# Kernel tuning notes

Hardware: AMD Instinct MI355X
Metric: run time of the kernel (lower is better)

The kernel has to match this reference:

```python
import jax, jax.numpy as jnp
import numpy as np

DIM = 1024
NUM_EXPERTS = 8
TOP_K = 2
HIDDEN = DIM * 2
B, S = 2, 4096


def setup_inputs() -> dict:
    key = jax.random.key(0)
    ks = jax.random.split(key, 8)
    sd = 1.0 / np.sqrt(DIM)
    sh = 1.0 / np.sqrt(HIDDEN)
    return {
        "x": jax.random.normal(ks[0], (B, S, DIM), dtype=jnp.float32),
        "gate_w": jax.random.uniform(ks[1], (NUM_EXPERTS, DIM), jnp.float32, -sd, sd),
        "gate_b": jax.random.uniform(ks[2], (NUM_EXPERTS,), jnp.float32, -sd, sd),
        "W1": jax.random.uniform(ks[3], (NUM_EXPERTS, DIM, HIDDEN), jnp.float32, -sd, sd),
        "b1": jax.random.uniform(ks[4], (NUM_EXPERTS, HIDDEN), jnp.float32, -sd, sd),
        "W2": jax.random.uniform(ks[5], (NUM_EXPERTS, HIDDEN, DIM), jnp.float32, -sh, sh),
        "b2": jax.random.uniform(ks[6], (NUM_EXPERTS, DIM), jnp.float32, -sh, sh),
    }


def reference(x, gate_w, gate_b, W1, b1, W2, b2):
    Bd, Sd, D = x.shape
    xf = x.reshape(-1, D)                                  # [T, D]
    T = xf.shape[0]
    logits = xf @ gate_w.T + gate_b                        # [T, E]
    weights = jax.nn.softmax(logits.astype(jnp.float32), axis=-1)
    topk_w, topk_i = jax.lax.top_k(weights, TOP_K)         # [T, K]
    topk_w = topk_w / topk_w.sum(axis=-1, keepdims=True)
    # combine weights scattered back to dense [T, E] (top-k indices are distinct)
    comb = jnp.zeros((T, NUM_EXPERTS), topk_w.dtype)
    comb = comb.at[jnp.arange(T)[:, None], topk_i].add(topk_w)
    # dense all-expert FFN (exact GELU, matching nn.GELU default)
    h = jax.nn.gelu(jnp.einsum('td,edh->eth', xf, W1) + b1[:, None, :], approximate=False)
    y = jnp.einsum('eth,ehd->etd', h, W2) + b2[:, None, :]  # [E, T, D]
    out = jnp.einsum('etd,te->td', y, comb.astype(y.dtype)).reshape(Bd, Sd, D)
    return out, logits
```

## Files before the change

### kernel.cpp

```cpp
#include <hip/hip_runtime.h>
#include <math.h>

#define T_TOK 8192
#define DIMX 1024
#define NE 8
#define HID 2048
#define NPAIR (T_TOK * 2)
#define P_PAD (NPAIR + NE * 128)
#define GATE_TPB 32

typedef __attribute__((ext_vector_type(8))) short s16x8;
typedef __attribute__((ext_vector_type(4))) float f32x4;

static __device__ __forceinline__ unsigned short f2bf(float f) {
    union { float f; unsigned u; } v; v.f = f;
    unsigned r = v.u + 0x7FFFu + ((v.u >> 16) & 1u);
    return (unsigned short)(r >> 16);
}
static __device__ __forceinline__ float bf2f(unsigned short u) {
    union { unsigned u; float f; } v; v.u = (unsigned)u << 16; return v.f;
}

static __device__ __forceinline__ float gelu_fast(float v) {
    float u2 = -1.5957691216057308f * v * (1.f + 0.044715f * v * v);
    return v * __builtin_amdgcn_rcpf(1.f + __expf(u2));
}

static __device__ __forceinline__ void gload16(const unsigned short* g, unsigned short* l) {
    __builtin_amdgcn_global_load_lds(
        (const __attribute__((address_space(1))) unsigned int*)g,
        (__attribute__((address_space(3))) unsigned int*)l, 16, 0, 0);
}

__global__ void init_routing_kernel(int* slot_token, float* slot_weight, int* counts) {
    int i = blockIdx.x * blockDim.x + threadIdx.x;
    if (i < P_PAD) { slot_token[i] = 0; slot_weight[i] = 0.f; }
    if (i < NE) counts[i] = 0;
}

__global__ __launch_bounds__(256) void conv_transpose_kernel(
    const float* __restrict__ src, unsigned short* __restrict__ dst, int R, int C) {
    __shared__ float tile[64][65];
    int e = blockIdx.z;
    int r0 = blockIdx.y * 64, c0 = blockIdx.x * 64;
    const float* s = src + (size_t)e * R * C;
    unsigned short* d = dst + (size_t)e * R * C;
    int tid = threadIdx.x;
    int lr = tid >> 4, lc4 = (tid & 15) * 4;
    #pragma unroll
    for (int it = 0; it < 4; it++) {
        float4 v = *(const float4*)&s[(size_t)(r0 + it * 16 + lr) * C + c0 + lc4];
        tile[it * 16 + lr][lc4 + 0] = v.x;
        tile[it * 16 + lr][lc4 + 1] = v.y;
        tile[it * 16 + lr][lc4 + 2] = v.z;
        tile[it * 16 + lr][lc4 + 3] = v.w;
    }
    __syncthreads();
    int cc = tid >> 3, rch = (tid & 7) * 8;
    #pragma unroll
    for (int it = 0; it < 2; it++) {
        int c = it * 32 + cc;
        unsigned short r[8];
        #pragma unroll
        for (int j = 0; j < 8; j++) r[j] = f2bf(tile[rch + j][c]);
        *(uint4*)&d[(size_t)(c0 + c) * R + r0 + rch] = *(const uint4*)&r[0];
    }
}

__global__ __launch_bounds__(256) void gate_kernel(
    const float* __restrict__ x, const float* __restrict__ gw, const float* __restrict__ gb,
    float* __restrict__ logits_out, int* counts, int* __restrict__ pair_epos,
    float* __restrict__ pair_w, unsigned short* __restrict__ xb) {
    __shared__ float sgw[NE * DIMX];
    __shared__ int lcount[NE], lbase[NE];
    __shared__ int s_e[GATE_TPB * 2];
    __shared__ int s_lp[GATE_TPB * 2];
    __shared__ float s_wv[GATE_TPB * 2];
    int tid = threadIdx.x;
    for (int i = tid; i < NE * DIMX / 4; i += 256)
        ((float4*)sgw)[i] = ((const float4*)gw)[i];
    if (tid < NE) lcount[tid] = 0;
    __syncthreads();

    int wave = tid >> 6, lane = tid & 63;
    int tbase = blockIdx.x * GATE_TPB;
    for (int r = 0; r < GATE_TPB / 4; ++r) {
        int ti = wave * (GATE_TPB / 4) + r;
        int t = tbase + ti;
        const float* xr = x + (size_t)t * DIMX;
        float acc[NE] = {};
        #pragma unroll
        for (int i = 0; i < DIMX / 256; i++) {
            float4 xv = *(const float4*)&xr[i * 256 + lane * 4];
            unsigned short rb[4] = { f2bf(xv.x), f2bf(xv.y), f2bf(xv.z), f2bf(xv.w) };
            *(uint2*)&xb[(size_t)t * DIMX + i * 256 + lane * 4] = *(const uint2*)&rb[0];
            #pragma unroll
            for (int e = 0; e < NE; e++) {
                float4 wv = *(const float4*)&sgw[e * DIMX + i * 256 + lane * 4];
                acc[e] += xv.x * wv.x + xv.y * wv.y + xv.z * wv.z + xv.w * wv.w;
            }
        }
        #pragma unroll
        for (int e = 0; e < NE; e++) {
            #pragma unroll
            for (int off = 32; off; off >>= 1) acc[e] += __shfl_xor(acc[e], off);
        }
        if (lane == 0) {
            float* lo = logits_out + (size_t)t * NE;
            #pragma unroll
            for (int e = 0; e < NE; e++) { acc[e] += gb[e]; lo[e] = acc[e]; }
            float l0 = acc[0]; int e0 = 0;
            #pragma unroll
            for (int e = 1; e < NE; e++) if (acc[e] > l0) { l0 = acc[e]; e0 = e; }
            float l1 = -1e30f; int e1 = -1;
            #pragma unroll
            for (int e = 0; e < NE; e++) if (e != e0 && acc[e] > l1) { l1 = acc[e]; e1 = e; }
            float q = expf(l1 - l0);
            float wn0 = 1.f / (1.f + q);
            float wn1 = q / (1.f + q);
            int lp0 = atomicAdd(&lcount[e0], 1);
            int lp1 = atomicAdd(&lcount[e1], 1);
            s_e[ti * 2] = e0; s_lp[ti * 2] = lp0; s_wv[ti * 2] = wn0;
            s_e[ti * 2 + 1] = e1; s_lp[ti * 2 + 1] = lp1; s_wv[ti * 2 + 1] = wn1;
        }
    }
    __syncthreads();
    if (tid < NE) lbase[tid] = atomicAdd(&counts[tid], lcount[tid]);
    __syncthreads();
    if (tid < GATE_TPB * 2) {
        int e = s_e[tid];
        int gp = lbase[e] + s_lp[tid];
        int gi = (tbase + (tid >> 1)) * 2 + (tid & 1);
        pair_epos[gi] = (e << 28) | gp;
        pair_w[gi] = s_wv[tid];
    }
}

__global__ void scan_kernel(const int* counts, int* offsets) {
    if (threadIdx.x == 0 && blockIdx.x == 0) {
        int o = 0;
        offsets[0] = 0;
        for (int e = 0; e < NE; e++) { o += (counts[e] + 127) & ~127; offsets[e + 1] = o; }
    }
}

__global__ void place_kernel(const int* __restrict__ pair_epos, const float* __restrict__ pair_w,
                             const int* __restrict__ offsets, int* __restrict__ slot_token,
                             float* __restrict__ slot_weight, int* __restrict__ tok2slot) {
    int p = blockIdx.x * 256 + threadIdx.x;
    if (p >= NPAIR) return;
    int ep = pair_epos[p];
    int e = ep >> 28;
    int pos = ep & 0x0FFFFFFF;
    int slot = offsets[e] + pos;
    slot_token[slot] = p >> 1;
    slot_weight[slot] = pair_w[p];
    tok2slot[p] = slot;
}

#define BARRIER() asm volatile("s_barrier" ::: "memory")
#define WAIT_VM(n) asm volatile("s_waitcnt vmcnt(" #n ")" ::: "memory")
#define WAIT_LGKM0() do { asm volatile("s_waitcnt lgkmcnt(0)" ::: "memory"); \
                          __builtin_amdgcn_sched_barrier(0); } while (0)


__global__ __launch_bounds__(256) void gemm1_kernel(
    const unsigned short* __restrict__ xb, const unsigned short* __restrict__ W1t,
    const float* __restrict__ b1, const int* __restrict__ offsets,
    const int* __restrict__ slot_token, unsigned short* __restrict__ hbuf) {
    int e = blockIdx.x;
    int row_base = offsets[e];
    int rows = offsets[e + 1] - row_base;
    int m0 = blockIdx.z * 128;
    if (m0 >= rows) return;
    int n0 = blockIdx.y * 128;

    __shared__ unsigned short sA[2][128 * 32];
    __shared__ unsigned short sB[2][128 * 32];

    int tid = threadIdx.x;
    const unsigned short* w1e = W1t + (size_t)e * HID * DIMX;

    int srow = tid >> 2;
    int kperm = (tid & 3) ^ ((tid >> 3) & 3);
    int tok0 = slot_token[row_base + m0 + srow];
    int tok1 = slot_token[row_base + m0 + srow + 64];
    const unsigned short* gA0 = xb + (size_t)tok0 * DIMX + kperm * 8;
    const unsigned short* gA1 = xb + (size_t)tok1 * DIMX + kperm * 8;
    const unsigned short* gB0 = w1e + (size_t)(n0 + srow) * DIMX + kperm * 8;
    const unsigned short* gB1 = w1e + (size_t)(n0 + srow + 64) * DIMX + kperm * 8;

#define STG1(b, k0) do { \
        gload16(gA0 + (k0), &sA[b][tid * 8]); \
        gload16(gA1 + (k0), &sA[b][(tid + 256) * 8]); \
        gload16(gB0 + (k0), &sB[b][tid * 8]); \
        gload16(gB1 + (k0), &sB[b][(tid + 256) * 8]); \
    } while (0)

    f32x4 acc[4][4] = {};
    int wv = tid >> 6; int wr = wv >> 1, wc = wv & 1;
    int lane = tid & 63; int lr = lane & 15, lg = lane >> 4;
    int kx8 = (lg ^ ((lr >> 1) & 3)) * 8;

#define CMP1(CUR) do { \
        s16x8 af[4], bfr[4]; \
        _Pragma("unroll") \
        for (int m = 0; m < 4; m++) af[m] = *(const s16x8*)&sA[CUR][(wr * 64 + m * 16 + lr) * 32 + kx8]; \
        _Pragma("unroll") \
        for (int n = 0; n < 4; n++) bfr[n] = *(const s16x8*)&sB[CUR][(wc * 64 + n * 16 + lr) * 32 + kx8]; \
        __builtin_amdgcn_s_setprio(1); \
        _Pragma("unroll") \
        for (int m = 0; m < 4; m++) { \
            _Pragma("unroll") \
            for (int n = 0; n < 4; n++) \
                acc[m][n] = __builtin_amdgcn_mfma_f32_16x16x32_bf16(af[m], bfr[n], acc[m][n], 0, 0, 0); \
        } \
        __builtin_amdgcn_s_setprio(0); \
    } while (0)

    const int NT = DIMX / 32;
    STG1(0, 0);
    int cur = 0;
    for (int t = 0; t < NT - 1; ++t) {
        STG1(cur ^ 1, (t + 1) * 32);
        WAIT_VM(4);
        BARRIER();
        CMP1(cur);
        WAIT_LGKM0();
        BARRIER();
        cur ^= 1;
    }
    WAIT_VM(0);
    BARRIER();
    CMP1(cur);
#undef STG1
#undef CMP1

    #pragma unroll
    for (int m = 0; m < 4; m++) {
        #pragma unroll
        for (int n = 0; n < 4; n++) {
            int col = n0 + wc * 64 + n * 16 + lr;
            float bias = b1[e * HID + col];
            #pragma unroll
            for (int i = 0; i < 4; i++) {
                int row = wr * 64 + m * 16 + lg * 4 + i;
                float v = gelu_fast(acc[m][n][i] + bias);
                hbuf[(size_t)(row_base + m0 + row) * HID + col] = f2bf(v);
            }
        }
    }
}

__global__ __launch_bounds__(256) void gemm2_kernel(
    const unsigned short* __restrict__ hbuf, const unsigned short* __restrict__ W2t,
    const float* __restrict__ b2, const int* __restrict__ offsets,
    const float* __restrict__ slot_weight, unsigned short* __restrict__ ybuf) {
    int e = blockIdx.x;
    int row_base = offsets[e];
    int rows = offsets[e + 1] - row_base;
    int m0 = blockIdx.z * 128;
    if (m0 >= rows) return;
    int n0 = blockIdx.y * 128;

    __shared__ unsigned short sA[2][128 * 32];
    __shared__ unsigned short sB[2][128 * 32];
    __shared__ float s_w[128];

    int tid = threadIdx.x;
    if (tid < 128) s_w[tid] = slot_weight[row_base + m0 + tid];

    const unsigned short* ha = hbuf + (size_t)(row_base + m0) * HID;
    const unsigned short* w2e = W2t + (size_t)e * DIMX * HID;

    int srow = tid >> 2;
    int kperm = (tid & 3) ^ ((tid >> 3) & 3);
    const unsigned short* gA0 = ha + (size_t)srow * HID + kperm * 8;
    const unsigned short* gA1 = ha + (size_t)(srow + 64) * HID + kperm * 8;
    const unsigned short* gB0 = w2e + (size_t)(n0 + srow) * HID + kperm * 8;
    const unsigned short* gB1 = w2e + (size_t)(n0 + srow + 64) * HID + kperm * 8;

#define STG2(b, k0) do { \
        gload16(gA0 + (k0), &sA[b][tid * 8]); \
        gload16(gA1 + (k0), &sA[b][(tid + 256) * 8]); \
        gload16(gB0 + (k0), &sB[b][tid * 8]); \
        gload16(gB1 + (k0), &sB[b][(tid + 256) * 8]); \
    } while (0)

    f32x4 acc[4][4] = {};
    int wv = tid >> 6; int wr = wv >> 1, wc = wv & 1;
    int lane = tid & 63; int lr = lane & 15, lg = lane >> 4;
    int kx8 = (lg ^ ((lr >> 1) & 3)) * 8;

#define CMP2(CUR) do { \
        s16x8 af[4], bfr[4]; \
        _Pragma("unroll") \
        for (int m = 0; m < 4; m++) af[m] = *(const s16x8*)&sA[CUR][(wr * 64 + m * 16 + lr) * 32 + kx8]; \
        _Pragma("unroll") \
        for (int n = 0; n < 4; n++) bfr[n] = *(const s16x8*)&sB[CUR][(wc * 64 + n * 16 + lr) * 32 + kx8]; \
        __builtin_amdgcn_s_setprio(1); \
        _Pragma("unroll") \
        for (int m = 0; m < 4; m++) { \
            _Pragma("unroll") \
            for (int n = 0; n < 4; n++) \
                acc[m][n] = __builtin_amdgcn_mfma_f32_16x16x32_bf16(af[m], bfr[n], acc[m][n], 0, 0, 0); \
        } \
        __builtin_amdgcn_s_setprio(0); \
    } while (0)

    const int NT = HID / 32;
    STG2(0, 0);
    int cur = 0;
    for (int t = 0; t < NT - 1; ++t) {
        STG2(cur ^ 1, (t + 1) * 32);
        WAIT_VM(4);
        BARRIER();
        CMP2(cur);
        WAIT_LGKM0();
        BARRIER();
        cur ^= 1;
    }
    WAIT_VM(0);
    BARRIER();
    CMP2(cur);
#undef STG2
#undef CMP2

    #pragma unroll
    for (int m = 0; m < 4; m++) {
        #pragma unroll
        for (int n = 0; n < 4; n++) {
            int col = n0 + wc * 64 + n * 16 + lr;
            float bias = b2[e * DIMX + col];
            #pragma unroll
            for (int i = 0; i < 4; i++) {
                int row = wr * 64 + m * 16 + lg * 4 + i;
                float v = (acc[m][n][i] + bias) * s_w[row];
                ybuf[(size_t)(row_base + m0 + row) * DIMX + col] = f2bf(v);
            }
        }
    }
}

__global__ __launch_bounds__(256) void combine_kernel(
    const unsigned short* __restrict__ ybuf, const int* __restrict__ tok2slot,
    float* __restrict__ out) {
    int t = blockIdx.x;
    int d = threadIdx.x * 4;
    int sa = tok2slot[t * 2], sb = tok2slot[t * 2 + 1];
    ushort4 a = *(const ushort4*)&ybuf[(size_t)sa * DIMX + d];
    ushort4 b = *(const ushort4*)&ybuf[(size_t)sb * DIMX + d];
    float4 o;
    o.x = bf2f(a.x) + bf2f(b.x);
    o.y = bf2f(a.y) + bf2f(b.y);
    o.z = bf2f(a.z) + bf2f(b.z);
    o.w = bf2f(a.w) + bf2f(b.w);
    *(float4*)&out[(size_t)t * DIMX + d] = o;
}

extern "C" void kernel_launch(void* const* d_in, const int* in_sizes, int n_in,
                              void* d_out, int out_size, void* d_ws, size_t ws_size,
                              hipStream_t stream) {
    const float* x  = (const float*)d_in[0];
    const float* gw = (const float*)d_in[1];
    const float* gb = (const float*)d_in[2];
    const float* W1 = (const float*)d_in[3];
    const float* b1 = (const float*)d_in[4];
    const float* W2 = (const float*)d_in[5];
    const float* b2 = (const float*)d_in[6];
    float* out = (float*)d_out;
    float* logits = out + (size_t)T_TOK * DIMX;

    char* ws = (char*)d_ws;
    unsigned short* W2t = (unsigned short*)ws; ws += (size_t)NE * DIMX * HID * 2;
    unsigned short* W1t = (unsigned short*)ws;
    unsigned short* ybuf = (unsigned short*)ws; ws += (size_t)NE * DIMX * HID * 2;
    unsigned short* xb = (unsigned short*)ws; ws += (size_t)T_TOK * DIMX * 2;
    unsigned short* hbuf = (unsigned short*)ws; ws += (size_t)P_PAD * HID * 2;
    int* counts = (int*)ws; ws += 256;
    int* offsets = (int*)ws; ws += 256;
    int* pair_epos = (int*)ws; ws += (size_t)NPAIR * 4;
    float* pair_w = (float*)ws; ws += (size_t)NPAIR * 4;
    int* slot_token = (int*)ws; ws += (size_t)P_PAD * 4;
    float* slot_weight = (float*)ws; ws += (size_t)P_PAD * 4;
    int* tok2slot = (int*)ws; ws += (size_t)NPAIR * 4;

    init_routing_kernel<<<(P_PAD + 255) / 256, 256, 0, stream>>>(slot_token, slot_weight, counts);
    conv_transpose_kernel<<<dim3(HID / 64, DIMX / 64, NE), 256, 0, stream>>>(W1, W1t, DIMX, HID);
    conv_transpose_kernel<<<dim3(DIMX / 64, HID / 64, NE), 256, 0, stream>>>(W2, W2t, HID, DIMX);
    gate_kernel<<<T_TOK / GATE_TPB, 256, 0, stream>>>(x, gw, gb, logits, counts, pair_epos,
                                                      pair_w, xb);
    scan_kernel<<<1, 1, 0, stream>>>(counts, offsets);
    place_kernel<<<NPAIR / 256, 256, 0, stream>>>(pair_epos, pair_w, offsets, slot_token,
                                                  slot_weight, tok2slot);
    gemm1_kernel<<<dim3(NE, HID / 128, 128), 256, 0, stream>>>(xb, W1t, b1, offsets, slot_token, hbuf);
    gemm2_kernel<<<dim3(NE, DIMX / 128, 128), 256, 0, stream>>>(hbuf, W2t, b2, offsets, slot_weight, ybuf);
    combine_kernel<<<T_TOK, 256, 0, stream>>>(ybuf, tok2slot, out);
}
```

Baseline: 281.0 us.

## Widen expert GEMM tiles to 128x256 with 512-thread blocks

Both grouped expert GEMMs now use 512-thread blocks of 8 waves arranged 2x4, each block computing a 128x256 output tile instead of 128x128. The A tile (tokens) is shared across twice as many output columns, which halves the A-operand global traffic and the number of blocks. The cost is more LDS per block (48KB double-buffered), fewer blocks for load balancing across experts with uneven row counts, and a launch-bounds hint of 4 that may constrain registers.

```diff
diff --git a/kernel.cpp b/kernel.cpp
--- a/kernel.cpp
+++ b/kernel.cpp
@@ -164,7 +164,7 @@
                           __builtin_amdgcn_sched_barrier(0); } while (0)
 
 
-__global__ __launch_bounds__(256) void gemm1_kernel(
+__global__ __launch_bounds__(512, 4) void gemm1_kernel(
     const unsigned short* __restrict__ xb, const unsigned short* __restrict__ W1t,
     const float* __restrict__ b1, const int* __restrict__ offsets,
     const int* __restrict__ slot_token, unsigned short* __restrict__ hbuf) {
@@ -173,32 +173,29 @@
     int rows = offsets[e + 1] - row_base;
     int m0 = blockIdx.z * 128;
     if (m0 >= rows) return;
-    int n0 = blockIdx.y * 128;
+    int n0 = blockIdx.y * 256;
 
     __shared__ unsigned short sA[2][128 * 32];
-    __shared__ unsigned short sB[2][128 * 32];
+    __shared__ unsigned short sB[2][256 * 32];
 
     int tid = threadIdx.x;
     const unsigned short* w1e = W1t + (size_t)e * HID * DIMX;
 
-    int srow = tid >> 2;
+    int arow = tid >> 2;
     int kperm = (tid & 3) ^ ((tid >> 3) & 3);
-    int tok0 = slot_token[row_base + m0 + srow];
-    int tok1 = slot_token[row_base + m0 + srow + 64];
-    const unsigned short* gA0 = xb + (size_t)tok0 * DIMX + kperm * 8;
-    const unsigned short* gA1 = xb + (size_t)tok1 * DIMX + kperm * 8;
-    const unsigned short* gB0 = w1e + (size_t)(n0 + srow) * DIMX + kperm * 8;
-    const unsigned short* gB1 = w1e + (size_t)(n0 + srow + 64) * DIMX + kperm * 8;
+    int tok = slot_token[row_base + m0 + arow];
+    const unsigned short* gA0 = xb + (size_t)tok * DIMX + kperm * 8;
+    const unsigned short* gB0 = w1e + (size_t)(n0 + arow) * DIMX + kperm * 8;
+    const unsigned short* gB1 = w1e + (size_t)(n0 + arow + 128) * DIMX + kperm * 8;
 
 #define STG1(b, k0) do { \
         gload16(gA0 + (k0), &sA[b][tid * 8]); \
-        gload16(gA1 + (k0), &sA[b][(tid + 256) * 8]); \
         gload16(gB0 + (k0), &sB[b][tid * 8]); \
-        gload16(gB1 + (k0), &sB[b][(tid + 256) * 8]); \
+        gload16(gB1 + (k0), &sB[b][tid * 8 + 4096]); \
     } while (0)
 
     f32x4 acc[4][4] = {};
-    int wv = tid >> 6; int wr = wv >> 1, wc = wv & 1;
+    int wid = tid >> 6; int wr = wid >> 2, wc = wid & 3;
     int lane = tid & 63; int lr = lane & 15, lg = lane >> 4;
     int kx8 = (lg ^ ((lr >> 1) & 3)) * 8;
 
@@ -223,7 +220,7 @@
     int cur = 0;
     for (int t = 0; t < NT - 1; ++t) {
         STG1(cur ^ 1, (t + 1) * 32);
-        WAIT_VM(4);
+        WAIT_VM(3);
         BARRIER();
         CMP1(cur);
         WAIT_LGKM0();
@@ -237,11 +234,11 @@
 #undef CMP1
 
     #pragma unroll
-    for (int m = 0; m < 4; m++) {
-        #pragma unroll
-        for (int n = 0; n < 4; n++) {
-            int col = n0 + wc * 64 + n * 16 + lr;
-            float bias = b1[e * HID + col];
+    for (int n = 0; n < 4; n++) {
+        int col = n0 + wc * 64 + n * 16 + lr;
+        float bias = b1[e * HID + col];
+        #pragma unroll
+        for (int m = 0; m < 4; m++) {
             #pragma unroll
             for (int i = 0; i < 4; i++) {
                 int row = wr * 64 + m * 16 + lg * 4 + i;
@@ -252,7 +249,7 @@
     }
 }
 
-__global__ __launch_bounds__(256) void gemm2_kernel(
+__global__ __launch_bounds__(512, 4) void gemm2_kernel(
     const unsigned short* __restrict__ hbuf, const unsigned short* __restrict__ W2t,
     const float* __restrict__ b2, const int* __restrict__ offsets,
     const float* __restrict__ slot_weight, unsigned short* __restrict__ ybuf) {
@@ -261,10 +258,10 @@
     int rows = offsets[e + 1] - row_base;
     int m0 = blockIdx.z * 128;
     if (m0 >= rows) return;
-    int n0 = blockIdx.y * 128;
+    int n0 = blockIdx.y * 256;
 
     __shared__ unsigned short sA[2][128 * 32];
-    __shared__ unsigned short sB[2][128 * 32];
+    __shared__ unsigned short sB[2][256 * 32];
     __shared__ float s_w[128];
 
     int tid = threadIdx.x;
@@ -273,22 +270,20 @@
     const unsigned short* ha = hbuf + (size_t)(row_base + m0) * HID;
     const unsigned short* w2e = W2t + (size_t)e * DIMX * HID;
 
-    int srow = tid >> 2;
+    int arow = tid >> 2;
     int kperm = (tid & 3) ^ ((tid >> 3) & 3);
-    const unsigned short* gA0 = ha + (size_t)srow * HID + kperm * 8;
-    const unsigned short* gA1 = ha + (size_t)(srow + 64) * HID + kperm * 8;
-    const unsigned short* gB0 = w2e + (size_t)(n0 + srow) * HID + kperm * 8;
-    const unsigned short* gB1 = w2e + (size_t)(n0 + srow + 64) * HID + kperm * 8;
+    const unsigned short* gA0 = ha + (size_t)arow * HID + kperm * 8;
+    const unsigned short* gB0 = w2e + (size_t)(n0 + arow) * HID + kperm * 8;
+    const unsigned short* gB1 = w2e + (size_t)(n0 + arow + 128) * HID + kperm * 8;
 
 #define STG2(b, k0) do { \
         gload16(gA0 + (k0), &sA[b][tid * 8]); \
-        gload16(gA1 + (k0), &sA[b][(tid + 256) * 8]); \
         gload16(gB0 + (k0), &sB[b][tid * 8]); \
-        gload16(gB1 + (k0), &sB[b][(tid + 256) * 8]); \
+        gload16(gB1 + (k0), &sB[b][tid * 8 + 4096]); \
     } while (0)
 
     f32x4 acc[4][4] = {};
-    int wv = tid >> 6; int wr = wv >> 1, wc = wv & 1;
+    int wid = tid >> 6; int wr = wid >> 2, wc = wid & 3;
     int lane = tid & 63; int lr = lane & 15, lg = lane >> 4;
     int kx8 = (lg ^ ((lr >> 1) & 3)) * 8;
 
@@ -313,7 +308,7 @@
     int cur = 0;
     for (int t = 0; t < NT - 1; ++t) {
         STG2(cur ^ 1, (t + 1) * 32);
-        WAIT_VM(4);
+        WAIT_VM(3);
         BARRIER();
         CMP2(cur);
         WAIT_LGKM0();
@@ -327,11 +322,11 @@
 #undef CMP2
 
     #pragma unroll
-    for (int m = 0; m < 4; m++) {
-        #pragma unroll
-        for (int n = 0; n < 4; n++) {
-            int col = n0 + wc * 64 + n * 16 + lr;
-            float bias = b2[e * DIMX + col];
+    for (int n = 0; n < 4; n++) {
+        int col = n0 + wc * 64 + n * 16 + lr;
+        float bias = b2[e * DIMX + col];
+        #pragma unroll
+        for (int m = 0; m < 4; m++) {
             #pragma unroll
             for (int i = 0; i < 4; i++) {
                 int row = wr * 64 + m * 16 + lg * 4 + i;
@@ -393,7 +388,7 @@
     scan_kernel<<<1, 1, 0, stream>>>(counts, offsets);
     place_kernel<<<NPAIR / 256, 256, 0, stream>>>(pair_epos, pair_w, offsets, slot_token,
                                                   slot_weight, tok2slot);
-    gemm1_kernel<<<dim3(NE, HID / 128, 128), 256, 0, stream>>>(xb, W1t, b1, offsets, slot_token, hbuf);
-    gemm2_kernel<<<dim3(NE, DIMX / 128, 128), 256, 0, stream>>>(hbuf, W2t, b2, offsets, slot_weight, ybuf);
+    gemm1_kernel<<<dim3(NE, HID / 256, 128), 512, 0, stream>>>(xb, W1t, b1, offsets, slot_token, hbuf);
+    gemm2_kernel<<<dim3(NE, DIMX / 256, 128), 512, 0, stream>>>(hbuf, W2t, b2, offsets, slot_weight, ybuf);
     combine_kernel<<<T_TOK, 256, 0, stream>>>(ybuf, tok2slot, out);
 }
```

Result: slower. 298.1 us (+6.1%).
